# Kernel optimization log

Measured on AMD Instinct MI355X. Metric: run time of the kernel, lower is better.

The kernel has to match this reference:

```python
import jax, jax.numpy as jnp
import numpy as np

E = 12000          # edge_num
D = 49 * 128       # sphere_basis_reduce * sphere_channels_reduce
H = 256            # hidden_channel
C = 128            # sphere_channels_reduce


def setup_inputs() -> dict:
    key = jax.random.key(0)
    ks = jax.random.split(key, 7)
    scale1 = 1.0 / np.sqrt(D)
    scale2 = 1.0 / np.sqrt(H)
    return {
        "node_embed": jax.random.normal(ks[0], (E, D), jnp.float32),
        "x_edge_c": jax.random.normal(ks[1], (E, H), jnp.float32),
        "ori": jax.random.normal(ks[2], (E, D), jnp.float32),
        "W1": jax.random.normal(ks[3], (D, H), jnp.float32) * scale1,
        "b1": jax.random.normal(ks[4], (H,), jnp.float32) * scale1,
        "W2": jax.random.normal(ks[5], (H, D), jnp.float32) * scale2,
        "b2": jax.random.normal(ks[6], (D,), jnp.float32) * scale2,
        "edge_num": E,
    }


def reference(node_embed, x_edge_c, ori, W1, b1, W2, b2, edge_num):
    # cat along edge axis: [2E, D]
    x = jnp.concatenate([node_embed, ori], axis=0)
    # fc1 + SiLU: [2E, H]
    h = jax.nn.silu(x @ W1 + b1)
    # edge-gated multiply, x_edge_c broadcast across the 2-way cat axis
    h = (h.reshape(2, edge_num, H) * x_edge_c.reshape(1, edge_num, H)).reshape(-1, H)
    # fc2 + SiLU: [2E, D]
    y = jax.nn.silu(h @ W2 + b2)
    # split-and-add combine: [E, D/C, C]
    y = y.reshape(2 * edge_num, -1, C)
    return y[:edge_num] + y[edge_num:]
```

## Files before the change

kernel.cpp:

```cpp
#include <hip/hip_runtime.h>

#define E_NUM 12000
#define D_DIM 6272
#define H_DIM 256
#define M1 24000

typedef __attribute__((ext_vector_type(8))) short short8;
typedef __attribute__((ext_vector_type(8))) __bf16 bf16x8;
typedef __attribute__((ext_vector_type(4))) float f32x4;

__device__ __forceinline__ float silu_f(float x) {
  return x / (1.0f + __expf(-x));
}

__device__ __forceinline__ bf16x8 ld_frag(const short* p) {
  return __builtin_bit_cast(bf16x8, *(const short8*)p);
}

__device__ __forceinline__ bf16x8 cvt8(f32x4 a, f32x4 b) {
  bf16x8 r;
#pragma unroll
  for (int j = 0; j < 4; ++j) {
    r[j] = (__bf16)a[j];
    r[4 + j] = (__bf16)b[j];
  }
  return r;
}

__device__ __forceinline__ void gll16(const void* g, void* l) {
  __builtin_amdgcn_global_load_lds(
      (const __attribute__((address_space(1))) void*)g,
      (__attribute__((address_space(3))) void*)l, 16, 0, 0);
}

__global__ void pack_p1(const float* __restrict__ W1, short* __restrict__ P1) {
  const int kt = blockIdx.x;
  const int col = threadIdx.x;
  const float* src = W1 + (size_t)kt * 32 * H_DIM + col;
  short* dst = P1 + ((size_t)kt * H_DIM + col) * 32;
#pragma unroll
  for (int c = 0; c < 4; ++c) {
    short8 s;
#pragma unroll
    for (int j = 0; j < 8; ++j)
      s[j] = __builtin_bit_cast(short, (__bf16)src[(size_t)(c * 8 + j) * H_DIM]);
    *(short8*)(dst + c * 8) = s;
  }
}

__global__ void pack_p2(const float* __restrict__ W2, short* __restrict__ P2) {
  const int kt = blockIdx.y;
  const int col = blockIdx.x * 128 + threadIdx.x;
  const float* src = W2 + (size_t)kt * 32 * D_DIM + col;
  short* dst = P2 + ((size_t)kt * D_DIM + col) * 32;
#pragma unroll
  for (int c = 0; c < 4; ++c) {
    short8 s;
#pragma unroll
    for (int j = 0; j < 8; ++j)
      s[j] = __builtin_bit_cast(short, (__bf16)src[(size_t)(c * 8 + j) * D_DIM]);
    *(short8*)(dst + c * 8) = s;
  }
}

#define G1_IT 196
__launch_bounds__(256, 3)
__global__ void gemm1_kernel(const float* __restrict__ node_embed,
                             const float* __restrict__ ori,
                             const float* __restrict__ x_edge_c,
                             const short* __restrict__ P1,
                             const float* __restrict__ b1,
                             short* __restrict__ hgp) {
  __shared__ __align__(16) float Als[2][64 * 32];
  __shared__ __align__(16) short Bls[2][256 * 32];

  const int t = threadIdx.x;
  const int wn = t >> 6;
  const int lane = t & 63;
  const int l15 = lane & 15;
  const int lq = lane >> 4;
  const int m_base = blockIdx.x * 64;

  const int sr = t >> 3;
  const int sgl = ((t >> 1) & 3) ^ (sr & 3);
  const int grow0 = m_base + sr;
  const int grow1 = m_base + sr + 32;
  const float* aAsrc = ((grow0 < E_NUM) ? node_embed + (size_t)grow0 * D_DIM
                                        : ori + (size_t)(grow0 - E_NUM) * D_DIM) +
                       sgl * 8 + (t & 1) * 4;
  const float* aBsrc = ((grow1 < E_NUM) ? node_embed + (size_t)grow1 * D_DIM
                                        : ori + (size_t)(grow1 - E_NUM) * D_DIM) +
                       sgl * 8 + (t & 1) * 4;

  const int bct = t >> 2;
  const int bgl = (t & 3) ^ (bct & 3);
  const short* bsrc = P1 + (size_t)bct * 32 + bgl * 8;

  const int axor = l15 & 3;

  f32x4 acc[4][4];
#pragma unroll
  for (int m = 0; m < 4; ++m)
#pragma unroll
    for (int n = 0; n < 4; ++n) acc[m][n] = (f32x4){0.f, 0.f, 0.f, 0.f};

  gll16(aAsrc, &Als[0][t * 4]);
  gll16(aBsrc, &Als[0][t * 4 + 1024]);
#pragma unroll
  for (int j = 0; j < 4; ++j) gll16(bsrc + j * 2048, &Bls[0][t * 8 + j * 2048]);
  __syncthreads();

  int cur = 0;
  for (int it = 0; it < G1_IT; ++it) {
    const int nxt = cur ^ 1;
    if (it + 1 < G1_IT) {
      const float* aa = aAsrc + (size_t)(it + 1) * 32;
      const float* ab = aBsrc + (size_t)(it + 1) * 32;
      gll16(aa, &Als[nxt][t * 4]);
      gll16(ab, &Als[nxt][t * 4 + 1024]);
      const short* bs = bsrc + (size_t)(it + 1) * 8192;
#pragma unroll
      for (int j = 0; j < 4; ++j) gll16(bs + j * 2048, &Bls[nxt][t * 8 + j * 2048]);
    }
    bf16x8 af[4];
    {
      const float* Ac = &Als[cur][0];
#pragma unroll
      for (int m = 0; m < 4; ++m) {
        const int ridx = (m * 16 + l15) * 32 + ((lq ^ axor) * 8);
        f32x4 lo = *(const f32x4*)(Ac + ridx);
        f32x4 hi = *(const f32x4*)(Ac + ridx + 4);
        af[m] = cvt8(lo, hi);
      }
    }
    bf16x8 bq[4];
#pragma unroll
    for (int n = 0; n < 4; ++n)
      bq[n] = ld_frag(&Bls[cur][(wn * 64 + n * 16 + l15) * 32 + ((lq ^ axor) * 8)]);
#pragma unroll
    for (int m = 0; m < 4; ++m)
#pragma unroll
      for (int n = 0; n < 4; ++n)
        acc[m][n] = __builtin_amdgcn_mfma_f32_16x16x32_bf16(af[m], bq[n], acc[m][n], 0, 0, 0);
    __syncthreads();
    cur = nxt;
  }

#pragma unroll
  for (int n = 0; n < 4; ++n) {
    const int col = wn * 64 + n * 16 + l15;
    const float b1v = b1[col];
    const int panel = wn * 2 + (n >> 1);
    const int cin = (n & 1) * 16 + l15;
#pragma unroll
    for (int m = 0; m < 4; ++m) {
#pragma unroll
      for (int i = 0; i < 4; ++i) {
        const int gmr = m_base + m * 16 + lq * 4 + i;
        const int e = (gmr < E_NUM) ? gmr : gmr - E_NUM;
        float v = acc[m][n][i] + b1v;
        v = silu_f(v) * x_edge_c[(size_t)e * H_DIM + col];
        hgp[((size_t)panel * M1 + gmr) * 32 + cin] = __builtin_bit_cast(short, (__bf16)v);
      }
    }
  }
}

__launch_bounds__(256, 4)
__global__ void gemm2_kernel(const short* __restrict__ hgp,
                             const short* __restrict__ P2,
                             const float* __restrict__ b2,
                             float* __restrict__ out) {
  __shared__ __align__(16) short Als2[2][128 * 32];
  __shared__ __align__(16) short Bls2[2][128 * 32];

  const int t = threadIdx.x;
  const int wd = t >> 6;
  const int lane = t & 63;
  const int l15 = lane & 15;
  const int lq = lane >> 4;
  const int d0 = blockIdx.x * 128;
  const int e0 = blockIdx.y * 64;

  const int sr = t >> 2;
  const int sgl = (t & 3) ^ (sr & 3);
  int eA = e0 + sr;
  if (eA >= E_NUM) eA = E_NUM - 1;
  const short* a0src = hgp + (size_t)eA * 32 + sgl * 8;
  const short* a1src = hgp + (size_t)(E_NUM + eA) * 32 + sgl * 8;
  const short* bsrc = P2 + (size_t)(d0 + sr) * 32 + sgl * 8;

  const int axor = l15 & 3;

  f32x4 acc[8][2];
#pragma unroll
  for (int m = 0; m < 8; ++m)
#pragma unroll
    for (int n = 0; n < 2; ++n) acc[m][n] = (f32x4){0.f, 0.f, 0.f, 0.f};

  gll16(a0src, &Als2[0][t * 8]);
  gll16(a1src, &Als2[0][t * 8 + 2048]);
  gll16(bsrc, &Bls2[0][t * 8]);
  gll16(bsrc + 2048, &Bls2[0][t * 8 + 2048]);
  __syncthreads();

  int cur = 0;
#pragma unroll
  for (int it = 0; it < 8; ++it) {
    const int nxt = cur ^ 1;
    if (it < 7) {
      const size_t ka = (size_t)(it + 1) * (M1 * 32);
      const size_t kb = (size_t)(it + 1) * ((size_t)D_DIM * 32);
      gll16(a0src + ka, &Als2[nxt][t * 8]);
      gll16(a1src + ka, &Als2[nxt][t * 8 + 2048]);
      gll16(bsrc + kb, &Bls2[nxt][t * 8]);
      gll16(bsrc + kb + 2048, &Bls2[nxt][t * 8 + 2048]);
    }
    bf16x8 bq[2];
#pragma unroll
    for (int n = 0; n < 2; ++n)
      bq[n] = ld_frag(&Bls2[cur][(wd * 32 + n * 16 + l15) * 32 + ((lq ^ axor) * 8)]);
#pragma unroll
    for (int m = 0; m < 8; ++m) {
      bf16x8 af = ld_frag(&Als2[cur][(m * 16 + l15) * 32 + ((lq ^ axor) * 8)]);
#pragma unroll
      for (int n = 0; n < 2; ++n)
        acc[m][n] = __builtin_amdgcn_mfma_f32_16x16x32_bf16(af, bq[n], acc[m][n], 0, 0, 0);
    }
    __syncthreads();
    cur = nxt;
  }

#pragma unroll
  for (int n = 0; n < 2; ++n) {
    const int col = d0 + wd * 32 + n * 16 + l15;
    const float b2v = b2[col];
#pragma unroll
    for (int mm = 0; mm < 4; ++mm) {
#pragma unroll
      for (int i = 0; i < 4; ++i) {
        const int e = e0 + mm * 16 + lq * 4 + i;
        if (e < E_NUM) {
          out[(size_t)e * D_DIM + col] =
              silu_f(acc[mm][n][i] + b2v) + silu_f(acc[mm + 4][n][i] + b2v);
        }
      }
    }
  }
}

extern "C" void kernel_launch(void* const* d_in, const int* in_sizes, int n_in,
                              void* d_out, int out_size, void* d_ws, size_t ws_size,
                              hipStream_t stream) {
  const float* node_embed = (const float*)d_in[0];
  const float* x_edge_c = (const float*)d_in[1];
  const float* ori = (const float*)d_in[2];
  const float* W1 = (const float*)d_in[3];
  const float* b1 = (const float*)d_in[4];
  const float* W2 = (const float*)d_in[5];
  const float* b2 = (const float*)d_in[6];
  float* out_p = (float*)d_out;

  char* ws = (char*)d_ws;
  short* P1 = (short*)ws;
  short* P2 = (short*)(ws + 3211264);
  short* hgp = (short*)(ws + 2 * 3211264);

  pack_p1<<<dim3(D_DIM / 32), 256, 0, stream>>>(W1, P1);
  pack_p2<<<dim3(D_DIM / 128, 8), 128, 0, stream>>>(W2, P2);

  gemm1_kernel<<<dim3(M1 / 64), 256, 0, stream>>>(node_embed, ori, x_edge_c, P1, b1, hgp);

  gemm2_kernel<<<dim3(D_DIM / 128, (E_NUM + 63) / 64), 256, 0, stream>>>(hgp, P2, b2, out_p);
}
```

Measured before the change: 507.1 us.

## Restructure both GEMMs: direct-global B fragments, smaller M tiles, full-K A staging

In gemm1, the M tile shrinks to 32 rows so twice as many blocks launch. K is staged 128 floats per step with an XOR swizzle, and the W1 fragments are read straight from global memory into registers instead of through LDS. In gemm2, the whole K=256 slice of the A rows (both halves) is loaded into LDS once, and B fragments come directly from global, which removes the per-K-step double buffering and barriers. This is meant to cut LDS traffic and synchronisation. In exchange it uses more registers, relies on cache hits for the global B loads, and lowers gemm2 occupancy through launch bounds of 2 and 64KB of LDS.

Result: faster. 466.7 us (-8.0%).

```diff
diff --git a/kernel.cpp b/kernel.cpp
--- a/kernel.cpp
+++ b/kernel.cpp
@@ -63,7 +63,7 @@
   }
 }
 
-#define G1_IT 196
+#define G1_NT 49
 __launch_bounds__(256, 3)
 __global__ void gemm1_kernel(const float* __restrict__ node_embed,
                              const float* __restrict__ ori,
@@ -71,77 +71,79 @@
                              const short* __restrict__ P1,
                              const float* __restrict__ b1,
                              short* __restrict__ hgp) {
-  __shared__ __align__(16) float Als[2][64 * 32];
-  __shared__ __align__(16) short Bls[2][256 * 32];
+  __shared__ __align__(16) float Abuf[2][32 * 128];
 
   const int t = threadIdx.x;
   const int wn = t >> 6;
   const int lane = t & 63;
   const int l15 = lane & 15;
   const int lq = lane >> 4;
-  const int m_base = blockIdx.x * 64;
-
-  const int sr = t >> 3;
-  const int sgl = ((t >> 1) & 3) ^ (sr & 3);
-  const int grow0 = m_base + sr;
-  const int grow1 = m_base + sr + 32;
-  const float* aAsrc = ((grow0 < E_NUM) ? node_embed + (size_t)grow0 * D_DIM
-                                        : ori + (size_t)(grow0 - E_NUM) * D_DIM) +
-                       sgl * 8 + (t & 1) * 4;
-  const float* aBsrc = ((grow1 < E_NUM) ? node_embed + (size_t)grow1 * D_DIM
-                                        : ori + (size_t)(grow1 - E_NUM) * D_DIM) +
-                       sgl * 8 + (t & 1) * 4;
-
-  const int bct = t >> 2;
-  const int bgl = (t & 3) ^ (bct & 3);
-  const short* bsrc = P1 + (size_t)bct * 32 + bgl * 8;
-
-  const int axor = l15 & 3;
-
-  f32x4 acc[4][4];
-#pragma unroll
-  for (int m = 0; m < 4; ++m)
+  const int m_base = blockIdx.x * 32;
+
+  const float* xb = (m_base < E_NUM) ? (node_embed + (size_t)m_base * D_DIM)
+                                     : (ori + (size_t)(m_base - E_NUM) * D_DIM);
+
+  const float* aP =
+      xb + (size_t)(t >> 5) * D_DIM + (((t & 24) | ((t & 7) ^ (t >> 5))) * 4);
+
+  const short* bbase = P1 + (size_t)(wn * 64 + l15) * 32 + lq * 8;
+
+  const int asw = l15 & 7;
+
+  f32x4 acc[2][4];
+#pragma unroll
+  for (int m = 0; m < 2; ++m)
 #pragma unroll
     for (int n = 0; n < 4; ++n) acc[m][n] = (f32x4){0.f, 0.f, 0.f, 0.f};
 
-  gll16(aAsrc, &Als[0][t * 4]);
-  gll16(aBsrc, &Als[0][t * 4 + 1024]);
-#pragma unroll
-  for (int j = 0; j < 4; ++j) gll16(bsrc + j * 2048, &Bls[0][t * 8 + j * 2048]);
+#define G1_STAGE(IT, BUF)                                                     \
+  do {                                                                        \
+    const float* _a = aP + (size_t)(IT)*128;                                  \
+    gll16(_a, &Abuf[BUF][t * 4]);                                             \
+    gll16(_a + (size_t)8 * D_DIM, &Abuf[BUF][t * 4 + 1024]);                  \
+    gll16(_a + (size_t)16 * D_DIM, &Abuf[BUF][t * 4 + 2048]);                 \
+    gll16(_a + (size_t)24 * D_DIM, &Abuf[BUF][t * 4 + 3072]);                 \
+  } while (0)
+
+  G1_STAGE(0, 0);
   __syncthreads();
 
   int cur = 0;
-  for (int it = 0; it < G1_IT; ++it) {
+  for (int it = 0; it < G1_NT; ++it) {
     const int nxt = cur ^ 1;
-    if (it + 1 < G1_IT) {
-      const float* aa = aAsrc + (size_t)(it + 1) * 32;
-      const float* ab = aBsrc + (size_t)(it + 1) * 32;
-      gll16(aa, &Als[nxt][t * 4]);
-      gll16(ab, &Als[nxt][t * 4 + 1024]);
-      const short* bs = bsrc + (size_t)(it + 1) * 8192;
-#pragma unroll
-      for (int j = 0; j < 4; ++j) gll16(bs + j * 2048, &Bls[nxt][t * 8 + j * 2048]);
-    }
-    bf16x8 af[4];
+
+    bf16x8 bq[4][4];
     {
-      const float* Ac = &Als[cur][0];
-#pragma unroll
-      for (int m = 0; m < 4; ++m) {
-        const int ridx = (m * 16 + l15) * 32 + ((lq ^ axor) * 8);
-        f32x4 lo = *(const f32x4*)(Ac + ridx);
-        f32x4 hi = *(const f32x4*)(Ac + ridx + 4);
+      const short* bs = bbase + (size_t)it * 32768;
+#pragma unroll
+      for (int ks = 0; ks < 4; ++ks)
+#pragma unroll
+        for (int n = 0; n < 4; ++n) bq[ks][n] = ld_frag(bs + ks * 8192 + n * 512);
+    }
+
+    if (it + 1 < G1_NT) G1_STAGE(it + 1, nxt);
+
+    const float* Ap = &Abuf[cur][0];
+#pragma unroll
+    for (int ks = 0; ks < 4; ++ks) {
+      bf16x8 af[2];
+#pragma unroll
+      for (int m = 0; m < 2; ++m) {
+        const int row = m * 16 + l15;
+        const int c_lo = 8 * ks + 2 * lq;
+        const int pl = (c_lo & 24) | ((c_lo & 7) ^ asw);
+        const int ph = (c_lo & 24) | (((c_lo + 1) & 7) ^ asw);
+        f32x4 lo = *(const f32x4*)(Ap + row * 128 + pl * 4);
+        f32x4 hi = *(const f32x4*)(Ap + row * 128 + ph * 4);
         af[m] = cvt8(lo, hi);
       }
-    }
-    bf16x8 bq[4];
-#pragma unroll
-    for (int n = 0; n < 4; ++n)
-      bq[n] = ld_frag(&Bls[cur][(wn * 64 + n * 16 + l15) * 32 + ((lq ^ axor) * 8)]);
-#pragma unroll
-    for (int m = 0; m < 4; ++m)
-#pragma unroll
-      for (int n = 0; n < 4; ++n)
-        acc[m][n] = __builtin_amdgcn_mfma_f32_16x16x32_bf16(af[m], bq[n], acc[m][n], 0, 0, 0);
+#pragma unroll
+      for (int m = 0; m < 2; ++m)
+#pragma unroll
+        for (int n = 0; n < 4; ++n)
+          acc[m][n] = __builtin_amdgcn_mfma_f32_16x16x32_bf16(af[m], bq[ks][n],
+                                                              acc[m][n], 0, 0, 0);
+    }
     __syncthreads();
     cur = nxt;
   }
@@ -153,7 +155,7 @@
     const int panel = wn * 2 + (n >> 1);
     const int cin = (n & 1) * 16 + l15;
 #pragma unroll
-    for (int m = 0; m < 4; ++m) {
+    for (int m = 0; m < 2; ++m) {
 #pragma unroll
       for (int i = 0; i < 4; ++i) {
         const int gmr = m_base + m * 16 + lq * 4 + i;
@@ -164,15 +166,15 @@
       }
     }
   }
-}
-
-__launch_bounds__(256, 4)
+#undef G1_STAGE
+}
+
+__launch_bounds__(256, 2)
 __global__ void gemm2_kernel(const short* __restrict__ hgp,
                              const short* __restrict__ P2,
                              const float* __restrict__ b2,
                              float* __restrict__ out) {
-  __shared__ __align__(16) short Als2[2][128 * 32];
-  __shared__ __align__(16) short Bls2[2][128 * 32];
+  __shared__ __align__(16) short Ah[128 * 256];
 
   const int t = threadIdx.x;
   const int wd = t >> 6;
@@ -182,15 +184,17 @@
   const int d0 = blockIdx.x * 128;
   const int e0 = blockIdx.y * 64;
 
-  const int sr = t >> 2;
-  const int sgl = (t & 3) ^ (sr & 3);
-  int eA = e0 + sr;
-  if (eA >= E_NUM) eA = E_NUM - 1;
-  const short* a0src = hgp + (size_t)eA * 32 + sgl * 8;
-  const short* a1src = hgp + (size_t)(E_NUM + eA) * 32 + sgl * 8;
-  const short* bsrc = P2 + (size_t)(d0 + sr) * 32 + sgl * 8;
-
-  const int axor = l15 & 3;
+  const int lc = (t & 24) | ((t & 7) ^ (t >> 5));
+#pragma unroll
+  for (int j = 0; j < 16; ++j) {
+    const int arow = j * 8 + (t >> 5);
+    int e = e0 + (arow & 63);
+    if (e >= E_NUM) e = E_NUM - 1;
+    const int grow = (arow < 64) ? e : (E_NUM + e);
+    const short* src = hgp + ((size_t)(lc >> 2) * M1 + grow) * 32 + (lc & 3) * 8;
+    gll16(src, &Ah[(j * 256 + t) * 8]);
+  }
+  __syncthreads();
 
   f32x4 acc[8][2];
 #pragma unroll
@@ -198,37 +202,23 @@
 #pragma unroll
     for (int n = 0; n < 2; ++n) acc[m][n] = (f32x4){0.f, 0.f, 0.f, 0.f};
 
-  gll16(a0src, &Als2[0][t * 8]);
-  gll16(a1src, &Als2[0][t * 8 + 2048]);
-  gll16(bsrc, &Bls2[0][t * 8]);
-  gll16(bsrc + 2048, &Bls2[0][t * 8 + 2048]);
-  __syncthreads();
-
-  int cur = 0;
-#pragma unroll
-  for (int it = 0; it < 8; ++it) {
-    const int nxt = cur ^ 1;
-    if (it < 7) {
-      const size_t ka = (size_t)(it + 1) * (M1 * 32);
-      const size_t kb = (size_t)(it + 1) * ((size_t)D_DIM * 32);
-      gll16(a0src + ka, &Als2[nxt][t * 8]);
-      gll16(a1src + ka, &Als2[nxt][t * 8 + 2048]);
-      gll16(bsrc + kb, &Bls2[nxt][t * 8]);
-      gll16(bsrc + kb + 2048, &Bls2[nxt][t * 8 + 2048]);
-    }
+  const int asw = l15 & 7;
+#pragma unroll
+  for (int kk = 0; kk < 8; ++kk) {
     bf16x8 bq[2];
 #pragma unroll
     for (int n = 0; n < 2; ++n)
-      bq[n] = ld_frag(&Bls2[cur][(wd * 32 + n * 16 + l15) * 32 + ((lq ^ axor) * 8)]);
+      bq[n] = ld_frag(P2 + (size_t)kk * ((size_t)D_DIM * 32) +
+                      (size_t)(d0 + wd * 32 + n * 16 + l15) * 32 + lq * 8);
 #pragma unroll
     for (int m = 0; m < 8; ++m) {
-      bf16x8 af = ld_frag(&Als2[cur][(m * 16 + l15) * 32 + ((lq ^ axor) * 8)]);
-#pragma unroll
-      for (int n = 0; n < 2; ++n)
-        acc[m][n] = __builtin_amdgcn_mfma_f32_16x16x32_bf16(af, bq[n], acc[m][n], 0, 0, 0);
-    }
-    __syncthreads();
-    cur = nxt;
+      const int row = (m & 3) * 16 + (m >> 2) * 64 + l15;
+      const int c = kk * 4 + lq;
+      const int pc = (c & 24) | ((c & 7) ^ asw);
+      bf16x8 af = ld_frag(&Ah[row * 256 + pc * 8]);
+      acc[m][0] = __builtin_amdgcn_mfma_f32_16x16x32_bf16(af, bq[0], acc[m][0], 0, 0, 0);
+      acc[m][1] = __builtin_amdgcn_mfma_f32_16x16x32_bf16(af, bq[1], acc[m][1], 0, 0, 0);
+    }
   }
 
 #pragma unroll
@@ -269,7 +259,7 @@
   pack_p1<<<dim3(D_DIM / 32), 256, 0, stream>>>(W1, P1);
   pack_p2<<<dim3(D_DIM / 128, 8), 128, 0, stream>>>(W2, P2);
 
-  gemm1_kernel<<<dim3(M1 / 64), 256, 0, stream>>>(node_embed, ori, x_edge_c, P1, b1, hgp);
+  gemm1_kernel<<<dim3(M1 / 32), 256, 0, stream>>>(node_embed, ori, x_edge_c, P1, b1, hgp);
 
   gemm2_kernel<<<dim3(D_DIM / 128, (E_NUM + 63) / 64), 256, 0, stream>>>(hgp, P2, b2, out_p);
 }
```
